# Kernel tuning notes

Measured on AMD Instinct MI355X. Metric: run time of the kernel, lower is better.

Reference implementation:

```python
import jax, jax.numpy as jnp
import numpy as np

D_IN = 512
D_OUT = 512
EPS = 1e-5


def setup_inputs() -> dict:
    key = jax.random.key(0)
    ks = jax.random.split(key, 6)
    B, T = 256, D_OUT + 1  # T includes CLS token (dropped in forward)
    x = jax.random.normal(ks[0], (B, T, D_IN), dtype=jnp.float32)
    s = 1.0 / np.sqrt(D_IN)
    W1 = jax.random.uniform(ks[1], (D_IN, D_IN), jnp.float32, -s, s)
    b1 = jax.random.uniform(ks[2], (D_IN,), jnp.float32, -s, s)
    gamma = jnp.ones((D_IN,), jnp.float32)
    beta = jnp.zeros((D_IN,), jnp.float32)
    Wout = jax.random.uniform(ks[3], (D_OUT, D_IN), jnp.float32, -s, s)  # stacked per-column Linear(d_in,1) weights
    bout = jax.random.uniform(ks[4], (D_OUT,), jnp.float32, -s, s)
    return {"x": x, "W1": W1, "b1": b1, "gamma": gamma, "beta": beta,
            "Wout": Wout, "bout": bout}


def reference(x, W1, b1, gamma, beta, Wout, bout):
    h = x[:, :-1]                              # drop CLS: [B, d_out, d_in]
    h = jnp.einsum('btd,ed->bte', h, W1) + b1  # linear1
    mu = jnp.mean(h, axis=-1, keepdims=True)
    var = jnp.mean(jnp.square(h - mu), axis=-1, keepdims=True)
    h = (h - mu) * jax.lax.rsqrt(var + EPS) * gamma + beta  # LayerNorm
    h = jax.nn.relu(h)
    # per-column head: out[:, t] = h[:, t] @ Wout[t] + bout[t]
    out = jnp.einsum('btd,td->bt', h, Wout) + bout  # [B, d_out]
    return out
```

## Files before the change

### kernel.cpp

```cpp
#include <hip/hip_runtime.h>


#define DIN     512
#define BK      32
#define MT      64
#define THREADS 512
#define NCHUNK  (DIN / BK)
#define ASTR    40
#define AS_SZ   (MT * ASTR)
#define BS_SZ   (DIN * BK)
#define BANDS   (BK * 16)

typedef __attribute__((ext_vector_type(8))) short bf16x8;
typedef __attribute__((ext_vector_type(4))) float f32x4;

__device__ __forceinline__ short f2bf(float f) {
    unsigned u = __float_as_uint(f);
    u = u + 0x7fffu + ((u >> 16) & 1u);
    return (short)(u >> 16);
}

__device__ __forceinline__ void gload_lds16(const void* g, void* l) {
    __builtin_amdgcn_global_load_lds(
        (const __attribute__((address_space(1))) unsigned int*)g,
        (__attribute__((address_space(3))) unsigned int*)l,
        16, 0, 0);
}

__global__ void cvt_w1_kernel(const float* __restrict__ w, short* __restrict__ o) {
    int i = blockIdx.x * blockDim.x + threadIdx.x;
    float4 v = ((const float4*)w)[i];
    short4 s;
    s.x = f2bf(v.x); s.y = f2bf(v.y); s.z = f2bf(v.z); s.w = f2bf(v.w);
    ((short4*)o)[i] = s;
}

__device__ __forceinline__ void stage_b_fallback(short* dstBuf, const float* W1f,
                                                 int c, int tid) {
    const float* src = W1f + (size_t)tid * DIN + c * BK;
    const int band = tid >> 4, rr = tid & 15;
    short* dstband = dstBuf + band * BANDS;
#pragma unroll
    for (int q = 0; q < 4; ++q) {
        float4 v0 = *(const float4*)(src + q * 8);
        float4 v1 = *(const float4*)(src + q * 8 + 4);
        int P = rr * 4 + (q ^ ((rr >> 1) & 3));
        short* d = dstband + P * 8;
        short4 s0, s1;
        s0.x = f2bf(v0.x); s0.y = f2bf(v0.y); s0.z = f2bf(v0.z); s0.w = f2bf(v0.w);
        s1.x = f2bf(v1.x); s1.y = f2bf(v1.y); s1.z = f2bf(v1.z); s1.w = f2bf(v1.w);
        *(short4*)d = s0;
        *(short4*)(d + 4) = s1;
    }
}

template<bool WS>
__global__ __launch_bounds__(THREADS, 4)
void fused_head_kernel(const float* __restrict__ x,
                       const float* __restrict__ W1f,
                       const short* __restrict__ W1h,
                       const float* __restrict__ b1,
                       const float* __restrict__ gamma,
                       const float* __restrict__ beta,
                       const float* __restrict__ Wout,
                       const float* __restrict__ bout,
                       float* __restrict__ out) {
    __shared__ __align__(16) short As[2][AS_SZ];
    __shared__ __align__(16) short Bs[2][BS_SZ];
    __shared__ float redS[MT][4];
    __shared__ float redQ[MT][4];
    __shared__ float meanA[MT];
    __shared__ float rstdA[MT];

    const int tid  = threadIdx.x;
    const int w    = tid >> 6;
    const int lane = tid & 63;
    const int q    = lane >> 4;
    const int l15  = lane & 15;
    const int rg   = w >> 2;
    const int cg   = w & 3;

    const int m0 = blockIdx.x * MT;
    const int bb = m0 >> 9;
    const int t0 = m0 & 511;
    const float* xbase = x + (size_t)(bb * 513 + t0) * DIN;

    const int ar = tid >> 3;
    const int ak = (tid & 7) * 4;

    const int brow = lane >> 2;
    const int bq   = (lane & 3) ^ ((lane >> 3) & 3);
    const short* bG = W1h + (size_t)(w * 64 + brow) * DIN + bq * 8;

    const int bOff = cg * (8 * BANDS)
                   + (l15 * 4 + (q ^ ((l15 >> 1) & 3))) * 8;

    f32x4 acc[2][8];
#pragma unroll
    for (int i = 0; i < 2; ++i)
#pragma unroll
        for (int j = 0; j < 8; ++j)
            acc[i][j] = (f32x4){0.f, 0.f, 0.f, 0.f};

    float4 aReg = *(const float4*)(xbase + ar * DIN + ak);
    if (WS) {
#pragma unroll
        for (int j = 0; j < 4; ++j)
            gload_lds16(bG + (size_t)(j * 16) * DIN,
                        &Bs[0][w * (4 * BANDS) + j * BANDS]);
    } else {
        stage_b_fallback(Bs[0], W1f, 0, tid);
    }
    {
        short4 a4;
        a4.x = f2bf(aReg.x); a4.y = f2bf(aReg.y);
        a4.z = f2bf(aReg.z); a4.w = f2bf(aReg.w);
        *(short4*)(&As[0][ar * ASTR + ak]) = a4;
    }
    aReg = *(const float4*)(xbase + ar * DIN + BK + ak);
    __syncthreads();

    for (int c = 0; c < NCHUNK; ++c) {
        const int cur = c & 1, nxt = cur ^ 1;

        if (c + 1 < NCHUNK) {
            if (WS) {
#pragma unroll
            for (int j = 0; j < 4; ++j)
                gload_lds16(bG + (size_t)(j * 16) * DIN + (c + 1) * BK,
                            &Bs[nxt][w * (4 * BANDS) + j * BANDS]);
            } else {
                stage_b_fallback(Bs[nxt], W1f, c + 1, tid);
            }
            short4 a4;
            a4.x = f2bf(aReg.x); a4.y = f2bf(aReg.y);
            a4.z = f2bf(aReg.z); a4.w = f2bf(aReg.w);
            *(short4*)(&As[nxt][ar * ASTR + ak]) = a4;
        }
        if (c + 2 < NCHUNK)
            aReg = *(const float4*)(xbase + ar * DIN + (c + 2) * BK + ak);

        const short* Ap = &As[cur][(rg * 32 + l15) * ASTR + q * 8];
        bf16x8 af0 = *(const bf16x8*)Ap;
        bf16x8 af1 = *(const bf16x8*)(Ap + 16 * ASTR);
        const short* Bp = &Bs[cur][bOff];
        {
            bf16x8 bfr[4];
#pragma unroll
            for (int tj = 0; tj < 4; ++tj)
                bfr[tj] = *(const bf16x8*)(Bp + tj * BANDS);
#pragma unroll
            for (int tj = 0; tj < 4; ++tj) {
                acc[0][tj] = __builtin_amdgcn_mfma_f32_16x16x32_bf16(
                    af0, bfr[tj], acc[0][tj], 0, 0, 0);
                acc[1][tj] = __builtin_amdgcn_mfma_f32_16x16x32_bf16(
                    af1, bfr[tj], acc[1][tj], 0, 0, 0);
            }
        }
        {
            bf16x8 bfr[4];
#pragma unroll
            for (int tj = 0; tj < 4; ++tj)
                bfr[tj] = *(const bf16x8*)(Bp + (tj + 4) * BANDS);
#pragma unroll
            for (int tj = 0; tj < 4; ++tj) {
                acc[0][tj + 4] = __builtin_amdgcn_mfma_f32_16x16x32_bf16(
                    af0, bfr[tj], acc[0][tj + 4], 0, 0, 0);
                acc[1][tj + 4] = __builtin_amdgcn_mfma_f32_16x16x32_bf16(
                    af1, bfr[tj], acc[1][tj + 4], 0, 0, 0);
            }
        }
        __syncthreads();
    }

    float b1v[8], gv[8], bv[8];
    const int cb = cg * 128 + l15;
#pragma unroll
    for (int tj = 0; tj < 8; ++tj) {
        int col = cb + tj * 16;
        b1v[tj] = b1[col];
        gv[tj]  = gamma[col];
        bv[tj]  = beta[col];
    }

#pragma unroll
    for (int ti = 0; ti < 2; ++ti)
#pragma unroll
        for (int r = 0; r < 4; ++r) {
            int row = rg * 32 + ti * 16 + q * 4 + r;
            float s = 0.f, s2 = 0.f;
#pragma unroll
            for (int tj = 0; tj < 8; ++tj) {
                float v = acc[ti][tj][r] + b1v[tj];
                s += v; s2 += v * v;
            }
#pragma unroll
            for (int m = 1; m < 16; m <<= 1) {
                s  += __shfl_xor(s,  m, 64);
                s2 += __shfl_xor(s2, m, 64);
            }
            if (l15 == 0) { redS[row][cg] = s; redQ[row][cg] = s2; }
        }
    __syncthreads();
    if (tid < MT) {
        float s  = redS[tid][0] + redS[tid][1] + redS[tid][2] + redS[tid][3];
        float s2 = redQ[tid][0] + redQ[tid][1] + redQ[tid][2] + redQ[tid][3];
        float mean = s * (1.f / DIN);
        float var  = s2 * (1.f / DIN) - mean * mean;
        meanA[tid] = mean;
        rstdA[tid] = rsqrtf(fmaxf(var, 0.f) + 1e-5f);
    }
    __syncthreads();

#pragma unroll
    for (int ti = 0; ti < 2; ++ti)
#pragma unroll
        for (int r = 0; r < 4; ++r) {
            int row = rg * 32 + ti * 16 + q * 4 + r;
            float mean = meanA[row], rs = rstdA[row];
            const float* wrow = Wout + (size_t)(t0 + row) * DIN + cb;
            float s = 0.f;
#pragma unroll
            for (int tj = 0; tj < 8; ++tj) {
                float v = acc[ti][tj][r] + b1v[tj];
                v = (v - mean) * rs * gv[tj] + bv[tj];
                v = fmaxf(v, 0.f);
                s += v * wrow[tj * 16];
            }
#pragma unroll
            for (int m = 1; m < 16; m <<= 1)
                s += __shfl_xor(s, m, 64);
            if (l15 == 0) redS[row][cg] = s;
        }
    __syncthreads();
    if (tid < MT)
        out[m0 + tid] = redS[tid][0] + redS[tid][1] + redS[tid][2] + redS[tid][3]
                        + bout[t0 + tid];
}

extern "C" void kernel_launch(void* const* d_in, const int* in_sizes, int n_in,
                              void* d_out, int out_size, void* d_ws, size_t ws_size,
                              hipStream_t stream) {
    const float* x     = (const float*)d_in[0];
    const float* W1    = (const float*)d_in[1];
    const float* b1    = (const float*)d_in[2];
    const float* gamma = (const float*)d_in[3];
    const float* beta  = (const float*)d_in[4];
    const float* Wout  = (const float*)d_in[5];
    const float* bout  = (const float*)d_in[6];
    float* out = (float*)d_out;

    const int M = 256 * 512;
    dim3 grid(M / MT), block(THREADS);

    if (ws_size >= (size_t)(DIN * DIN) * sizeof(short)) {
        short* W1h = (short*)d_ws;
        cvt_w1_kernel<<<DIN * DIN / (256 * 4), 256, 0, stream>>>(W1, W1h);
        fused_head_kernel<true><<<grid, block, 0, stream>>>(
            x, W1, W1h, b1, gamma, beta, Wout, bout, out);
    } else {
        fused_head_kernel<false><<<grid, block, 0, stream>>>(
            x, W1, nullptr, b1, gamma, beta, Wout, bout, out);
    }
}
```

Measured before the change: 437.0 us.

## Split B-tile staging into half-chunk loads with fine-grained vmcnt waits and barriers

The W1 tile is now staged in two halves: columns 0-255 and 256-511, with interleaved column ownership across wave groups. A mid-iteration barrier lets the second-half loads for the next chunk be issued after the first half of the MFMAs has consumed its data. Block-wide __syncthreads are replaced by explicit s_waitcnt vmcnt counts plus s_barrier, so outstanding global-to-LDS loads can overlap compute. The epilogue column mapping changes to match the new interleaving. This adds a second barrier per chunk and relies on exact vmcnt accounting, which is fragile; the final iteration also issues a redundant load of the last chunk.

```diff
diff --git a/kernel.cpp b/kernel.cpp
--- a/kernel.cpp
+++ b/kernel.cpp
@@ -90,10 +90,9 @@
 
     const int brow = lane >> 2;
     const int bq   = (lane & 3) ^ ((lane >> 3) & 3);
-    const short* bG = W1h + (size_t)(w * 64 + brow) * DIN + bq * 8;
-
-    const int bOff = cg * (8 * BANDS)
-                   + (l15 * 4 + (q ^ ((l15 >> 1) & 3))) * 8;
+    const short* bGw = W1h + (size_t)(32 * w + brow) * DIN + bq * 8;
+
+    const int bU = (l15 * 4 + (q ^ ((l15 >> 1) & 3))) * 8;
 
     f32x4 acc[2][8];
 #pragma unroll
@@ -105,9 +104,14 @@
     float4 aReg = *(const float4*)(xbase + ar * DIN + ak);
     if (WS) {
 #pragma unroll
-        for (int j = 0; j < 4; ++j)
-            gload_lds16(bG + (size_t)(j * 16) * DIN,
-                        &Bs[0][w * (4 * BANDS) + j * BANDS]);
+        for (int j = 0; j < 2; ++j)
+            gload_lds16(bGw + (size_t)(16 * j) * DIN,
+                        &Bs[0][(2 * w + j) * BANDS]);
+#pragma unroll
+        for (int j = 0; j < 2; ++j)
+            gload_lds16(bGw + (size_t)(256 + 16 * j) * DIN,
+                        &Bs[0][(16 + 2 * w + j) * BANDS]);
+        __builtin_amdgcn_sched_barrier(0);
     } else {
         stage_b_fallback(Bs[0], W1f, 0, tid);
     }
@@ -117,38 +121,37 @@
         a4.z = f2bf(aReg.z); a4.w = f2bf(aReg.w);
         *(short4*)(&As[0][ar * ASTR + ak]) = a4;
     }
-    aReg = *(const float4*)(xbase + ar * DIN + BK + ak);
-    __syncthreads();
+    if (WS) {
+        asm volatile("s_waitcnt vmcnt(2) lgkmcnt(0)" ::: "memory");
+        __builtin_amdgcn_sched_barrier(0);
+        __builtin_amdgcn_s_barrier();
+    } else {
+        __syncthreads();
+    }
 
     for (int c = 0; c < NCHUNK; ++c) {
         const int cur = c & 1, nxt = cur ^ 1;
-
-        if (c + 1 < NCHUNK) {
-            if (WS) {
-#pragma unroll
-            for (int j = 0; j < 4; ++j)
-                gload_lds16(bG + (size_t)(j * 16) * DIN + (c + 1) * BK,
-                            &Bs[nxt][w * (4 * BANDS) + j * BANDS]);
-            } else {
-                stage_b_fallback(Bs[nxt], W1f, c + 1, tid);
-            }
-            short4 a4;
-            a4.x = f2bf(aReg.x); a4.y = f2bf(aReg.y);
-            a4.z = f2bf(aReg.z); a4.w = f2bf(aReg.w);
-            *(short4*)(&As[nxt][ar * ASTR + ak]) = a4;
-        }
-        if (c + 2 < NCHUNK)
-            aReg = *(const float4*)(xbase + ar * DIN + (c + 2) * BK + ak);
-
+        const int cn = (c + 1 < NCHUNK) ? c + 1 : NCHUNK - 1;
+
+        aReg = *(const float4*)(xbase + ar * DIN + cn * BK + ak);
+        __builtin_amdgcn_sched_barrier(0);
+        if (WS) {
+#pragma unroll
+            for (int j = 0; j < 2; ++j)
+                gload_lds16(bGw + (size_t)(16 * j) * DIN + cn * BK,
+                            &Bs[nxt][(2 * w + j) * BANDS]);
+            __builtin_amdgcn_sched_barrier(0);
+        } else if (c + 1 < NCHUNK) {
+            stage_b_fallback(Bs[nxt], W1f, c + 1, tid);
+        }
         const short* Ap = &As[cur][(rg * 32 + l15) * ASTR + q * 8];
         bf16x8 af0 = *(const bf16x8*)Ap;
         bf16x8 af1 = *(const bf16x8*)(Ap + 16 * ASTR);
-        const short* Bp = &Bs[cur][bOff];
         {
             bf16x8 bfr[4];
 #pragma unroll
             for (int tj = 0; tj < 4; ++tj)
-                bfr[tj] = *(const bf16x8*)(Bp + tj * BANDS);
+                bfr[tj] = *(const bf16x8*)(&Bs[cur][(tj * 4 + cg) * BANDS + bU]);
 #pragma unroll
             for (int tj = 0; tj < 4; ++tj) {
                 acc[0][tj] = __builtin_amdgcn_mfma_f32_16x16x32_bf16(
@@ -157,11 +160,32 @@
                     af1, bfr[tj], acc[1][tj], 0, 0, 0);
             }
         }
+        if (WS) {
+            asm volatile("s_waitcnt vmcnt(3) lgkmcnt(0)" ::: "memory");
+            __builtin_amdgcn_sched_barrier(0);
+            __builtin_amdgcn_s_barrier();
+        } else {
+            __syncthreads();
+        }
+
+        if (WS) {
+#pragma unroll
+            for (int j = 0; j < 2; ++j)
+                gload_lds16(bGw + (size_t)(256 + 16 * j) * DIN + cn * BK,
+                            &Bs[nxt][(16 + 2 * w + j) * BANDS]);
+            __builtin_amdgcn_sched_barrier(0);
+        }
+        {
+            short4 a4;
+            a4.x = f2bf(aReg.x); a4.y = f2bf(aReg.y);
+            a4.z = f2bf(aReg.z); a4.w = f2bf(aReg.w);
+            *(short4*)(&As[nxt][ar * ASTR + ak]) = a4;
+        }
         {
             bf16x8 bfr[4];
 #pragma unroll
             for (int tj = 0; tj < 4; ++tj)
-                bfr[tj] = *(const bf16x8*)(Bp + (tj + 4) * BANDS);
+                bfr[tj] = *(const bf16x8*)(&Bs[cur][(16 + tj * 4 + cg) * BANDS + bU]);
 #pragma unroll
             for (int tj = 0; tj < 4; ++tj) {
                 acc[0][tj + 4] = __builtin_amdgcn_mfma_f32_16x16x32_bf16(
@@ -170,14 +194,20 @@
                     af1, bfr[tj], acc[1][tj + 4], 0, 0, 0);
             }
         }
-        __syncthreads();
+        if (WS) {
+            asm volatile("s_waitcnt vmcnt(2) lgkmcnt(0)" ::: "memory");
+            __builtin_amdgcn_sched_barrier(0);
+            __builtin_amdgcn_s_barrier();
+        } else {
+            __syncthreads();
+        }
     }
 
     float b1v[8], gv[8], bv[8];
-    const int cb = cg * 128 + l15;
+    const int cb = cg * 16 + l15;
 #pragma unroll
     for (int tj = 0; tj < 8; ++tj) {
-        int col = cb + tj * 16;
+        int col = tj * 64 + cb;
         b1v[tj] = b1[col];
         gv[tj]  = gamma[col];
         bv[tj]  = beta[col];
@@ -225,7 +255,7 @@
                 float v = acc[ti][tj][r] + b1v[tj];
                 v = (v - mean) * rs * gv[tj] + bv[tj];
                 v = fmaxf(v, 0.f);
-                s += v * wrow[tj * 16];
+                s += v * wrow[tj * 64];
             }
 #pragma unroll
             for (int m = 1; m < 16; m <<= 1)
```

Result: slower. 460.1 us (+5.3%).
